# Optimization experiments

Measured on AMD Instinct MI355X. Metric: run time of the kernel, lower is better.

The kernel has to match this reference:

```python
import jax, jax.numpy as jnp
import numpy as np

H = 256      # hidden_dim
MEL = 80     # num_mel
R = 5        # reduction_factor
BS = 128
T_ENC = 512
T_DEC = 1000


def _gru_step(x, h, wih, whh, bih, bhh):
    # PyTorch GRU cell: gates order (r, z, n)
    gi = x @ wih.T + bih            # [bs, 3H]
    gh = h @ whh.T + bhh
    ir, iz, inn = jnp.split(gi, 3, axis=-1)
    hr, hz, hn = jnp.split(gh, 3, axis=-1)
    r = jax.nn.sigmoid(ir + hr)
    z = jax.nn.sigmoid(iz + hz)
    n = jnp.tanh(inn + r * hn)
    return (1.0 - z) * n + z * h


def setup_inputs() -> dict:
    key = jax.random.key(0)
    ks = iter(jax.random.split(key, 40))
    s = 0.05
    def w(shape):
        return jax.random.normal(next(ks), shape, dtype=jnp.float32) * s
    inp = {
        "enc_vec": jax.random.normal(next(ks), (BS, T_ENC, H), dtype=jnp.float32),
        "decoder_input": jax.random.normal(next(ks), (BS, T_DEC, MEL), dtype=jnp.float32),
        # Pre_net
        "pre_w1": w((H, MEL)), "pre_b1": jnp.zeros((H,), jnp.float32),
        "pre_w2": w((H // 2, H)), "pre_b2": jnp.zeros((H // 2,), jnp.float32),
        # Bahdanau attention
        "w1": w((H, H)), "b1": jnp.zeros((H,), jnp.float32),
        "w2": w((H, H)), "b2": jnp.zeros((H,), jnp.float32),
        "v_w": w((1, H)), "v_b": jnp.zeros((1,), jnp.float32),
        # projection and output
        "proj_w": w((H, 2 * H)), "proj_b": jnp.zeros((H,), jnp.float32),
        "out_w": w((MEL * R, H)), "out_b": jnp.zeros((MEL * R,), jnp.float32),
        # Attention GRU (input H//2)
        "att_wih": w((3 * H, H // 2)), "att_whh": w((3 * H, H)),
        "att_bih": jnp.zeros((3 * H,), jnp.float32), "att_bhh": jnp.zeros((3 * H,), jnp.float32),
        # GRU1, GRU2 (input H)
        "g1_wih": w((3 * H, H)), "g1_whh": w((3 * H, H)),
        "g1_bih": jnp.zeros((3 * H,), jnp.float32), "g1_bhh": jnp.zeros((3 * H,), jnp.float32),
        "g2_wih": w((3 * H, H)), "g2_whh": w((3 * H, H)),
        "g2_bih": jnp.zeros((3 * H,), jnp.float32), "g2_bhh": jnp.zeros((3 * H,), jnp.float32),
    }
    return inp


def reference(enc_vec, decoder_input, pre_w1, pre_b1, pre_w2, pre_b2,
              w1, b1, w2, b2, v_w, v_b, proj_w, proj_b, out_w, out_b,
              att_wih, att_whh, att_bih, att_bhh,
              g1_wih, g1_whh, g1_bih, g1_bhh,
              g2_wih, g2_whh, g2_bih, g2_bhh):
    bs = enc_vec.shape[0]
    # Pre_net (dropout omitted -> deterministic eval behavior)
    pre = jax.nn.relu(decoder_input @ pre_w1.T + pre_b1)
    pre = jax.nn.relu(pre @ pre_w2.T + pre_b2)          # [bs, T_dec, H//2]
    steps = decoder_input.shape[1] // R                 # 200
    # teacher-forced inputs: step i uses pre[:, i*R, :]
    xs = jnp.transpose(pre[:, :steps * R:R, :], (1, 0, 2))   # [steps, bs, H//2]
    # hoist W1(enc_vec): constant across decoder steps
    w1enc = enc_vec @ w1.T + b1                         # [bs, T_enc, H]

    h0 = jnp.zeros((bs, H), jnp.float32)

    def step(carry, x):
        ha, h1, h2 = carry
        d = _gru_step(x, ha, att_wih, att_whh, att_bih, att_bhh)   # [bs, H]
        e = jnp.tanh(w1enc + (d @ w2.T + b2)[:, None, :])          # [bs, T_enc, H]
        scores = e @ v_w[0] + v_b[0]                               # [bs, T_enc]
        u = jax.nn.softmax(scores, axis=1)
        d_dot = jnp.einsum('bt,bth->bh', u, enc_vec)               # [bs, H]
        p = jnp.concatenate([d, d_dot], axis=-1) @ proj_w.T + proj_b  # [bs, H]
        o1 = _gru_step(p, h1, g1_wih, g1_whh, g1_bih, g1_bhh)
        in2 = o1 + p
        o2 = _gru_step(in2, h2, g2_wih, g2_whh, g2_bih, g2_bhh)
        out = (in2 + o2) @ out_w.T + out_b                         # [bs, R*MEL]
        return (d, o1, o2), out

    _, ys = jax.lax.scan(step, (h0, h0, h0), xs)        # [steps, bs, R*MEL]
    ys = jnp.transpose(ys, (1, 0, 2)).reshape(bs, steps * R, MEL)
    return ys
```

## Files before the change

### kernel.cpp

```cpp
#include <hip/hip_runtime.h>
#include <hip/hip_bf16.h>

typedef unsigned short u16;
typedef unsigned int   u32;

constexpr int H     = 256;
constexpr int HH    = 128;
constexpr int MELD  = 80;
constexpr int RF    = 5;
constexpr int BS    = 128;
constexpr int TENC  = 512;
constexpr int TDEC  = 1000;
constexpr int STEPS = 200;
constexpr int OD    = 400;
constexpr int M_ALL = STEPS * BS;

constexpr size_t GI_B   = 0;
constexpr size_t ENC16_B= GI_B;
constexpr size_t D16_B  = GI_B   + (size_t)M_ALL*768*4;
constexpr size_t IN2_B  = D16_B;
constexpr size_t W1ET_B = D16_B  + (size_t)M_ALL*512*2;
constexpr size_t P16_B  = W1ET_B;
constexpr size_t IN2H_B = W1ET_B + (size_t)M_ALL*256*2;
constexpr size_t P_B    = W1ET_B + (size_t)BS*H*TENC*2;
constexpr size_t U16_B  = P_B;
constexpr size_t XSH_B  = P_B    + (size_t)M_ALL*256*4;
constexpr size_t ST16_B = XSH_B  + (size_t)M_ALL*128*2;
constexpr size_t WPK_B  = ST16_B + (size_t)M_ALL*256*2;
constexpr size_t WH_B   = WPK_B  + 3*(size_t)393216;
constexpr size_t WH_AW  = 0;
constexpr size_t WH_W2  = WH_AW + 98304*2;
constexpr size_t WH_PJ  = WH_W2 + 65536*2;
constexpr size_t WH_G1  = WH_PJ + 131072*2;
constexpr size_t WH_G2  = WH_G1 + 196608*2;
constexpr size_t WH_OW  = WH_G2 + 196608*2;
constexpr size_t WH_W1  = WH_OW + 102400*2;
constexpr size_t WH_END = WH_W1 + 65536*2;
constexpr size_t NEED_FAST = WH_B + WH_END;

constexpr size_t FBW1E_B  = 65536;
constexpr size_t FBXST_B  = FBW1E_B + (size_t)BS*TENC*H*2;
constexpr size_t FBF32_B  = FBXST_B + (size_t)STEPS*HH*BS*2;
constexpr size_t FBDT_F   = 0;
constexpr size_t FBO1_F   = FBDT_F + 2*(size_t)H*BS;
constexpr size_t FBO2_F   = FBO1_F + 2*(size_t)H*BS;
constexpr size_t FBPT_F   = FBO2_F + 2*(size_t)H*BS;
constexpr size_t FBIN2_F  = FBPT_F + (size_t)H*BS;
constexpr size_t FBST_F   = FBIN2_F + (size_t)H*BS;
constexpr size_t FB_NEED_B = FBF32_B + (FBST_F + 2*(size_t)H*BS) * 4;

__device__ __forceinline__ float bf2f(u16 v) {
  union { u32 x; float f; } c; c.x = ((u32)v) << 16; return c.f;
}
__device__ __forceinline__ float bfu_lo(u32 u) { union { u32 x; float f; } c; c.x = u << 16;        return c.f; }
__device__ __forceinline__ float bfu_hi(u32 u) { union { u32 x; float f; } c; c.x = u & 0xffff0000u; return c.f; }
__device__ __forceinline__ u16 f2bf(float f) {
  union { float f; u32 u; } c; c.f = f;
  u32 u = c.u;
  u32 r = (u + 0x7fffu + ((u >> 16) & 1u)) >> 16;
  return (u16)r;
}
__device__ __forceinline__ u16 f2h(float f) {
  union { _Float16 h; u16 u; } c; c.h = (_Float16)f; return c.u;
}
__device__ __forceinline__ float fexp(float x) {
  return __builtin_amdgcn_exp2f(1.4426950408889634f * x);
}
__device__ __forceinline__ float sigm_f(float x) {
  return __builtin_amdgcn_rcpf(1.0f + __builtin_amdgcn_exp2f(-1.4426950408889634f * x));
}
__device__ __forceinline__ float tanh_f(float x) {
  x = fminf(fmaxf(x, -15.f), 15.f);
  float e = __builtin_amdgcn_exp2f(2.8853900817779268f * x);
  return (e - 1.0f) * __builtin_amdgcn_rcpf(e + 1.0f);
}

typedef _Float16 hlf2 __attribute__((ext_vector_type(2)));
typedef _Float16 f16x8 __attribute__((ext_vector_type(8)));
typedef float f32x4 __attribute__((ext_vector_type(4)));
#if __has_builtin(__builtin_amdgcn_fdot2)
__device__ __forceinline__ float dot2h(float acc, u32 w, u32 h) {
  union { u32 u; hlf2 v; } cw, ch; cw.u = w; ch.u = h;
  return __builtin_amdgcn_fdot2(cw.v, ch.v, acc, false);
}
#else
__device__ __forceinline__ float dot2h(float acc, u32 w, u32 h) {
  union { u32 u; _Float16 f[2]; } cw, ch; cw.u = w; ch.u = h;
  return acc + (float)cw.f[0] * (float)ch.f[0] + (float)cw.f[1] * (float)ch.f[1];
}
#endif
__device__ __forceinline__ void dot8h(float& acc, const uint4 w, const uint4 hp) {
  acc = dot2h(acc, w.x, hp.x);
  acc = dot2h(acc, w.y, hp.y);
  acc = dot2h(acc, w.z, hp.z);
  acc = dot2h(acc, w.w, hp.w);
}

__global__ __launch_bounds__(256) void k_zero(float* __restrict__ out, int n) {
  int i = blockIdx.x * 256 + threadIdx.x;
  if (i < n) out[i] = 0.f;
}


__global__ __launch_bounds__(256) void k_prenet_f(
    const float* __restrict__ dec, const float* __restrict__ w1, const float* __restrict__ b1,
    const float* __restrict__ w2, const float* __restrict__ b2, u16* __restrict__ xsh)
{
  const int s = blockIdx.x, tid = threadIdx.x;
  __shared__ float X0[32][80];
  __shared__ float P1t[32][256];
  for (int bt = 0; bt < 4; ++bt) {
    const int b0 = bt * 32;
    __syncthreads();
    for (int i = tid; i < 32 * 80; i += 256) {
      int bb = i / 80, m = i - bb * 80;
      X0[bb][m] = dec[((size_t)(b0 + bb) * TDEC + (size_t)s * RF) * MELD + m];
    }
    __syncthreads();
    {
      const int h = tid;
      float acc[32];
      const float bias = b1[h];
      #pragma unroll
      for (int r = 0; r < 32; ++r) acc[r] = bias;
      const float* wr = w1 + (size_t)h * MELD;
      for (int m = 0; m < 80; m += 4) {
        float4 wv = *(const float4*)(wr + m);
        #pragma unroll
        for (int r = 0; r < 32; ++r) {
          float4 x = *(const float4*)&X0[r][m];
          acc[r] += x.x * wv.x + x.y * wv.y + x.z * wv.z + x.w * wv.w;
        }
      }
      #pragma unroll
      for (int r = 0; r < 32; ++r) P1t[r][h] = fmaxf(acc[r], 0.f);
    }
    __syncthreads();
    {
      const int k = tid & 127, bh = tid >> 7;
      float acc[16];
      const float bias = b2[k];
      #pragma unroll
      for (int r = 0; r < 16; ++r) acc[r] = bias;
      const float* wr = w2 + (size_t)k * H;
      for (int h = 0; h < H; h += 4) {
        float4 wv = *(const float4*)(wr + h);
        #pragma unroll
        for (int r = 0; r < 16; ++r) {
          float4 x = *(const float4*)&P1t[bh * 16 + r][h];
          acc[r] += x.x * wv.x + x.y * wv.y + x.z * wv.z + x.w * wv.w;
        }
      }
      #pragma unroll
      for (int r = 0; r < 16; ++r)
        xsh[((size_t)s * BS + b0 + bh * 16 + r) * HH + k] = f2h(fmaxf(acc[r], 0.f));
    }
  }
}

__global__ __launch_bounds__(256) void k_packall(
    const float* __restrict__ enc, u16* __restrict__ enc16,
    const float* __restrict__ awhh, const float* __restrict__ g1whh,
    const float* __restrict__ g2whh, u32* __restrict__ wpk,
    const float* __restrict__ awih, u16* __restrict__ awih16,
    const float* __restrict__ w2w,  u16* __restrict__ w2w16,
    const float* __restrict__ pjw,  u16* __restrict__ pjw16,
    const float* __restrict__ g1wih, u16* __restrict__ g1w16,
    const float* __restrict__ g2wih, u16* __restrict__ g2w16,
    const float* __restrict__ ow,   u16* __restrict__ ow16,
    const float* __restrict__ w1w,  u16* __restrict__ w1w16)
{
  int i = blockIdx.x * 256 + threadIdx.x;
  if (i < 16777216) { enc16[i] = f2h(enc[i]); return; }
  i -= 16777216;
  if (i < 294912) {
    int which = i / 98304, idx = i - which * 98304;
    const float* w = which == 0 ? awhh : (which == 1 ? g1whh : g2whh);
    int ii = idx & 3;
    int j  = (idx >> 2) & 255;
    int k4 = (idx >> 10) & 31;
    int g  = idx >> 15;
    int k2 = 4 * k4 + ii;
    union { _Float16 f[2]; u32 u; } c;
    c.f[0] = (_Float16)w[((size_t)g * 256 + j) * 256 + 2 * k2];
    c.f[1] = (_Float16)w[((size_t)g * 256 + j) * 256 + 2 * k2 + 1];
    wpk[which * 98304 + idx] = c.u;
    return;
  }
  i -= 294912;
  if (i < 98304)  { awih16[i] = f2h(awih[i]); return; }  i -= 98304;
  if (i < 65536)  { w2w16[i]  = f2h(w2w[i]);  return; }  i -= 65536;
  if (i < 131072) { pjw16[i]  = f2h(pjw[i]);  return; }  i -= 131072;
  if (i < 196608) { g1w16[i]  = f2h(g1wih[i]); return; } i -= 196608;
  if (i < 196608) { g2w16[i]  = f2h(g2wih[i]); return; } i -= 196608;
  if (i < 102400) { ow16[i]   = f2h(ow[i]);   return; }  i -= 102400;
  if (i < 65536)  { w1w16[i]  = f2h(w1w[i]);  return; }
}
constexpr int PACKALL_N = 16777216 + 294912 + 856064;

__global__ __launch_bounds__(256) void k_hgemm(
    const u16* __restrict__ A, int lda,
    const u16* __restrict__ W, int K,
    const float* __restrict__ bias,
    float* __restrict__ C, u16* __restrict__ Ch, int ldc, int N,
    float* __restrict__ outmap, u16* __restrict__ CbfT)
{
  __shared__ _Float16 As[128 * 40];
  __shared__ _Float16 Ws[64 * 40];
  const int m0 = blockIdx.y * 128, n0 = blockIdx.x * 64;
  const int tid = threadIdx.x;
  const int wv = tid >> 6, lane = tid & 63;
  const int l15 = lane & 15, hi = lane >> 4;
  f32x4 acc[2][4];
  #pragma unroll
  for (int mi = 0; mi < 2; ++mi)
    #pragma unroll
    for (int ni = 0; ni < 4; ++ni) acc[mi][ni] = (f32x4){0.f, 0.f, 0.f, 0.f};

  const int ar = tid >> 1, ac = (tid & 1) * 16;
  const int wr = tid >> 2, wc = (tid & 3) * 8;
  for (int k0 = 0; k0 < K; k0 += 32) {
    __syncthreads();
    {
      const u16* src = A + (size_t)(m0 + ar) * lda + k0 + ac;
      uint4 v0 = *(const uint4*)(src);
      uint4 v1 = *(const uint4*)(src + 8);
      *(uint4*)&As[ar * 40 + ac] = v0;
      *(uint4*)&As[ar * 40 + ac + 8] = v1;
    }
    {
      uint4 v;
      if (n0 + wr < N) v = *(const uint4*)(W + (size_t)(n0 + wr) * K + k0 + wc);
      else { v.x = v.y = v.z = v.w = 0u; }
      *(uint4*)&Ws[wr * 40 + wc] = v;
    }
    __syncthreads();
    f16x8 af[2], bf[4];
    #pragma unroll
    for (int mi = 0; mi < 2; ++mi)
      af[mi] = *(const f16x8*)&As[(wv * 32 + mi * 16 + l15) * 40 + hi * 8];
    #pragma unroll
    for (int ni = 0; ni < 4; ++ni)
      bf[ni] = *(const f16x8*)&Ws[(ni * 16 + l15) * 40 + hi * 8];
    #pragma unroll
    for (int mi = 0; mi < 2; ++mi)
      #pragma unroll
      for (int ni = 0; ni < 4; ++ni)
        acc[mi][ni] = __builtin_amdgcn_mfma_f32_16x16x32_f16(af[mi], bf[ni], acc[mi][ni], 0, 0, 0);
  }
  const int gm = m0 + wv * 32;
  #pragma unroll
  for (int ni = 0; ni < 4; ++ni) {
    const int col = n0 + ni * 16 + l15;
    if (col < N) {
      const float bv = bias[col];
      #pragma unroll
      for (int mi = 0; mi < 2; ++mi) {
        #pragma unroll
        for (int r = 0; r < 4; ++r) {
          const int row = gm + mi * 16 + hi * 4 + r;
          float v = acc[mi][ni][r] + bv;
          if (outmap) {
            int s = row >> 7, b = row & 127;
            int fr = s * RF + col / MELD, mel = col - (col / MELD) * MELD;
            outmap[((size_t)b * TDEC + fr) * MELD + mel] = v;
          } else if (CbfT) {
            float a = fminf(fmaxf(2.8853900817779268f * v, -15.f), 15.f);
            CbfT[(((size_t)(row >> 9) * 256 + col) << 9) + (row & 511)] =
                f2bf(__builtin_amdgcn_exp2f(a));
          } else {
            if (C)  C[(size_t)row * ldc + col] = v;
            if (Ch) Ch[(size_t)row * ldc + col] = f2h(v);
          }
        }
      }
    }
  }
}

__global__ __launch_bounds__(256) void k_ddgemm(
    const u16* __restrict__ U, const float* __restrict__ enc,
    u16* __restrict__ D16)
{
  __shared__ _Float16 As[128 * 40];
  __shared__ _Float16 Ws[64 * 40];
  const int b = blockIdx.z;
  const int m0 = blockIdx.y * 128, n0 = blockIdx.x * 64;
  const int tid = threadIdx.x;
  const int wv = tid >> 6, lane = tid & 63;
  const int l15 = lane & 15, hi = lane >> 4;
  f32x4 acc[2][4];
  #pragma unroll
  for (int mi = 0; mi < 2; ++mi)
    #pragma unroll
    for (int ni = 0; ni < 4; ++ni) acc[mi][ni] = (f32x4){0.f, 0.f, 0.f, 0.f};

  const u16* A = U + (size_t)b * STEPS * TENC;
  const float* E = enc + (size_t)b * TENC * H;
  const int ar = tid >> 1, ac = (tid & 1) * 16;
  for (int k0 = 0; k0 < TENC; k0 += 32) {
    __syncthreads();
    {
      const u16* src = A + (size_t)(m0 + ar) * TENC + k0 + ac;
      uint4 v0 = *(const uint4*)(src);
      uint4 v1 = *(const uint4*)(src + 8);
      *(uint4*)&As[ar * 40 + ac] = v0;
      *(uint4*)&As[ar * 40 + ac + 8] = v1;
    }
    {
      #pragma unroll
      for (int it = 0; it < 2; ++it) {
        int flat = tid + it * 256;
        int kk = flat >> 4, hc4 = (flat & 15) * 4;
        float4 v = *(const float4*)(E + (size_t)(k0 + kk) * H + n0 + hc4);
        Ws[(hc4 + 0) * 40 + kk] = (_Float16)v.x;
        Ws[(hc4 + 1) * 40 + kk] = (_Float16)v.y;
        Ws[(hc4 + 2) * 40 + kk] = (_Float16)v.z;
        Ws[(hc4 + 3) * 40 + kk] = (_Float16)v.w;
      }
    }
    __syncthreads();
    f16x8 af[2], bf[4];
    #pragma unroll
    for (int mi = 0; mi < 2; ++mi)
      af[mi] = *(const f16x8*)&As[(wv * 32 + mi * 16 + l15) * 40 + hi * 8];
    #pragma unroll
    for (int ni = 0; ni < 4; ++ni)
      bf[ni] = *(const f16x8*)&Ws[(ni * 16 + l15) * 40 + hi * 8];
    #pragma unroll
    for (int mi = 0; mi < 2; ++mi)
      #pragma unroll
      for (int ni = 0; ni < 4; ++ni)
        acc[mi][ni] = __builtin_amdgcn_mfma_f32_16x16x32_f16(af[mi], bf[ni], acc[mi][ni], 0, 0, 0);
  }
  const int gm = m0 + wv * 32;
  #pragma unroll
  for (int ni = 0; ni < 4; ++ni) {
    const int col = n0 + ni * 16 + l15;
    #pragma unroll
    for (int mi = 0; mi < 2; ++mi) {
      #pragma unroll
      for (int r = 0; r < 4; ++r) {
        const int row = gm + mi * 16 + hi * 4 + r;
        if (row < STEPS)
          D16[((size_t)(row * BS + b)) * 512 + 256 + col] = f2h(acc[mi][ni][r]);
      }
    }
  }
}

constexpr int KC4H = 2;
constexpr int RG4H = 14;
__global__ __launch_bounds__(512) void k_chain(
    const float* __restrict__ gi,
    const uint4* __restrict__ wpk4,
    const float* __restrict__ bhh,
    const float* __restrict__ addsrc,
    int astride,
    float* __restrict__ outp, int ostride,
    u16* __restrict__ outph, int ostrideh)
{
  const int b = blockIdx.x, tid = threadIdx.x;
  const int j = tid & 255, kh = tid >> 8;
  __shared__ __align__(16) _Float16 hf[256];
  __shared__ float psum[3][256];
  __shared__ uint4 wl4[3][2 * KC4H][256];
  for (int i = tid; i < 3 * 2 * KC4H * 256; i += 512) {
    int g = i / (2 * KC4H * 256), rem = i - g * (2 * KC4H * 256);
    int slot = rem >> 8, jj = rem & 255;
    int c = slot < KC4H ? slot : slot - KC4H;
    int k4 = (slot < KC4H ? 0 : 16) + c;
    wl4[g][slot][jj] = wpk4[((size_t)g * 32 + k4) * 256 + jj];
  }
  uint4 wreg[3][RG4H];
  #pragma unroll
  for (int g = 0; g < 3; ++g) {
    #pragma unroll
    for (int t = 0; t < RG4H; ++t) {
      const int k4 = kh * 16 + KC4H + t;
      wreg[g][t] = wpk4[((size_t)g * 32 + k4) * 256 + j];
    }
  }
  if (tid < 256) hf[tid] = (_Float16)0.f;
  float hreg = 0.f;
  const float br = bhh[j], bz = bhh[256 + j], bn = bhh[512 + j];
  float gr = 0.f, gz = 0.f, gn = 0.f, av = 0.f;
  if (kh == 0) {
    const float* gim = gi + (size_t)b * 768;
    gr = gim[j]; gz = gim[256 + j]; gn = gim[512 + j];
    if (addsrc) av = addsrc[(size_t)b * astride + j];
  }
  __syncthreads();
  for (int s = 0; s < STEPS; ++s) {
    float gr_n = 0.f, gz_n = 0.f, gn_n = 0.f, av_n = 0.f;
    if (kh == 0 && s + 1 < STEPS) {
      const size_t mn = (size_t)(s + 1) * BS + b;
      const float* gim = gi + mn * 768;
      gr_n = gim[j]; gz_n = gim[256 + j]; gn_n = gim[512 + j];
      if (addsrc) av_n = addsrc[mn * astride + j];
    }
    float ar = 0.f, az = 0.f, an = 0.f;
    const int k4b = kh * 16;
    #pragma unroll
    for (int t = 0; t < RG4H; ++t) {
      const int k4 = k4b + KC4H + t;
      uint4 hp = *(const uint4*)&hf[8 * k4];
      dot8h(ar, wreg[0][t], hp); dot8h(az, wreg[1][t], hp); dot8h(an, wreg[2][t], hp);
    }
    #pragma unroll
    for (int c = 0; c < KC4H; ++c) {
      const int k4 = k4b + c;
      const int slot = kh * KC4H + c;
      uint4 hp = *(const uint4*)&hf[8 * k4];
      dot8h(ar, wl4[0][slot][j], hp); dot8h(az, wl4[1][slot][j], hp); dot8h(an, wl4[2][slot][j], hp);
    }
    if (kh == 1) { psum[0][j] = ar; psum[1][j] = az; psum[2][j] = an; }
    __syncthreads();
    if (kh == 0) {
      const size_t m = (size_t)s * BS + b;
      ar += psum[0][j]; az += psum[1][j]; an += psum[2][j];
      float r = sigm_f(gr + ar + br);
      float z = sigm_f(gz + az + bz);
      float n = tanh_f(gn + r * (an + bn));
      float hn_ = (1.f - z) * n + z * hreg;
      hreg = hn_;
      hf[j] = (_Float16)hn_;
      float ov = hn_ + av;
      if (outp)  outp[m * ostride + j] = ov;
      if (outph) outph[m * ostrideh + j] = f2h(ov);
    }
    __syncthreads();
    gr = gr_n; gz = gz_n; gn = gn_n; av = av_n;
  }
}

constexpr int ATT_ST = 10;
__global__ __launch_bounds__(256) void k_att(
    const u16* __restrict__ w1eT, const float* __restrict__ Q,
    const float* __restrict__ vw_, u16* __restrict__ U16)
{
  const int b = blockIdx.x, s0 = blockIdx.y * ATT_ST, tid = threadIdx.x;
  __shared__ float qt[ATT_ST][260];
  __shared__ float vws[256];
  __shared__ float redw[ATT_ST][4];
  vws[tid] = -2.0f * vw_[tid];
  #pragma unroll
  for (int si = 0; si < ATT_ST; ++si) {
    float q = 2.8853900817779268f * Q[((size_t)(s0 + si) * BS + b) * H + tid];
    qt[si][tid] = __builtin_amdgcn_exp2f(fminf(fmaxf(q, -15.f), 15.f));
  }
  __syncthreads();

  float sc0[ATT_ST], sc1[ATT_ST];
  #pragma unroll
  for (int si = 0; si < ATT_ST; ++si) { sc0[si] = 0.f; sc1[si] = 0.f; }
  const u32* wrow = (const u32*)w1eT + (size_t)b * H * (TENC / 2);
  for (int h = 0; h < H; h += 4) {
    u32 wa = wrow[(size_t)(h + 0) * 256 + tid];
    u32 wb = wrow[(size_t)(h + 1) * 256 + tid];
    u32 wc = wrow[(size_t)(h + 2) * 256 + tid];
    u32 wd = wrow[(size_t)(h + 3) * 256 + tid];
    float Ea0 = bfu_lo(wa), Ea1 = bfu_hi(wa);
    float Eb0 = bfu_lo(wb), Eb1 = bfu_hi(wb);
    float Ec0 = bfu_lo(wc), Ec1 = bfu_hi(wc);
    float Ed0 = bfu_lo(wd), Ed1 = bfu_hi(wd);
    float4 vv = *(const float4*)&vws[h];
    #pragma unroll
    for (int si = 0; si < ATT_ST; ++si) {
      float4 Eq = *(const float4*)&qt[si][h];
      {
        float F1 = __builtin_fmaf(Ea0, Eq.x, 1.f);
        float F2 = __builtin_fmaf(Eb0, Eq.y, 1.f);
        float F3 = __builtin_fmaf(Ec0, Eq.z, 1.f);
        float F4 = __builtin_fmaf(Ed0, Eq.w, 1.f);
        float P12 = F1 * F2, P34 = F3 * F4;
        float u12 = __builtin_fmaf(vv.y, F1, vv.x * F2);
        float u34 = __builtin_fmaf(vv.w, F3, vv.z * F4);
        float num = __builtin_fmaf(P12, u34, P34 * u12);
        sc0[si] = __builtin_fmaf(num, __builtin_amdgcn_rcpf(P12 * P34), sc0[si]);
      }
      {
        float F1 = __builtin_fmaf(Ea1, Eq.x, 1.f);
        float F2 = __builtin_fmaf(Eb1, Eq.y, 1.f);
        float F3 = __builtin_fmaf(Ec1, Eq.z, 1.f);
        float F4 = __builtin_fmaf(Ed1, Eq.w, 1.f);
        float P12 = F1 * F2, P34 = F3 * F4;
        float u12 = __builtin_fmaf(vv.y, F1, vv.x * F2);
        float u34 = __builtin_fmaf(vv.w, F3, vv.z * F4);
        float num = __builtin_fmaf(P12, u34, P34 * u12);
        sc1[si] = __builtin_fmaf(num, __builtin_amdgcn_rcpf(P12 * P34), sc1[si]);
      }
    }
  }
  const int lane = tid & 63, wvi = tid >> 6;
  #pragma unroll
  for (int si = 0; si < ATT_ST; ++si) {
    float mw = fmaxf(sc0[si], sc1[si]);
    for (int off = 1; off < 64; off <<= 1) mw = fmaxf(mw, __shfl_xor(mw, off));
    if (lane == 0) redw[si][wvi] = mw;
  }
  __syncthreads();
  #pragma unroll
  for (int si = 0; si < ATT_ST; ++si) {
    float mx = fmaxf(fmaxf(redw[si][0], redw[si][1]), fmaxf(redw[si][2], redw[si][3]));
    sc0[si] = fexp(sc0[si] - mx);
    sc1[si] = fexp(sc1[si] - mx);
  }
  __syncthreads();
  #pragma unroll
  for (int si = 0; si < ATT_ST; ++si) {
    float sm = sc0[si] + sc1[si];
    for (int off = 1; off < 64; off <<= 1) sm += __shfl_xor(sm, off);
    if (lane == 0) redw[si][wvi] = sm;
  }
  __syncthreads();
  #pragma unroll
  for (int si = 0; si < ATT_ST; ++si) {
    float tot = redw[si][0] + redw[si][1] + redw[si][2] + redw[si][3];
    float li = __builtin_amdgcn_rcpf(tot);
    u32 pk = (u32)f2h(sc0[si] * li) | ((u32)f2h(sc1[si] * li) << 16);
    *(u32*)&U16[((size_t)b * STEPS + s0 + si) * TENC + 2 * tid] = pk;
  }
}

__global__ __launch_bounds__(256) void fbk_zeroinit(float* __restrict__ fst) {
  int i = blockIdx.x * 256 + threadIdx.x;
  if (i < H * BS)              fst[FBDT_F + i] = 0.f;
  else if (i < 2 * H * BS)     fst[FBO1_F + (i - H * BS)] = 0.f;
  else if (i < 3 * H * BS)     fst[FBO2_F + (i - 2 * H * BS)] = 0.f;
}

__global__ __launch_bounds__(256) void fbk_prenet(
    const float* __restrict__ dec, const float* __restrict__ w1, const float* __restrict__ b1,
    const float* __restrict__ w2, const float* __restrict__ b2, u16* __restrict__ xsT)
{
  const int s = blockIdx.x, tid = threadIdx.x;
  __shared__ float X0[32][80];
  __shared__ float P1t[32][256];
  for (int bt = 0; bt < 4; ++bt) {
    const int b0 = bt * 32;
    __syncthreads();
    for (int i = tid; i < 32 * 80; i += 256) {
      int bb = i / 80, m = i - bb * 80;
      X0[bb][m] = dec[((size_t)(b0 + bb) * TDEC + (size_t)s * RF) * MELD + m];
    }
    __syncthreads();
    {
      const int h = tid;
      float acc[32];
      const float bias = b1[h];
      #pragma unroll
      for (int r = 0; r < 32; ++r) acc[r] = bias;
      const float* wr = w1 + (size_t)h * MELD;
      for (int m = 0; m < 80; m += 4) {
        float4 wv = *(const float4*)(wr + m);
        #pragma unroll
        for (int r = 0; r < 32; ++r) {
          float4 x = *(const float4*)&X0[r][m];
          acc[r] += x.x * wv.x + x.y * wv.y + x.z * wv.z + x.w * wv.w;
        }
      }
      #pragma unroll
      for (int r = 0; r < 32; ++r) P1t[r][h] = fmaxf(acc[r], 0.f);
    }
    __syncthreads();
    {
      const int k = tid & 127, bh = tid >> 7;
      float acc[16];
      const float bias = b2[k];
      #pragma unroll
      for (int r = 0; r < 16; ++r) acc[r] = bias;
      const float* wr = w2 + (size_t)k * H;
      for (int h = 0; h < H; h += 4) {
        float4 wv = *(const float4*)(wr + h);
        #pragma unroll
        for (int r = 0; r < 16; ++r) {
          float4 x = *(const float4*)&P1t[bh * 16 + r][h];
          acc[r] += x.x * wv.x + x.y * wv.y + x.z * wv.z + x.w * wv.w;
        }
      }
      #pragma unroll
      for (int r = 0; r < 16; ++r)
        xsT[((size_t)s * HH + k) * BS + b0 + bh * 16 + r] = f2bf(fmaxf(acc[r], 0.f));
    }
  }
}

__global__ __launch_bounds__(256) void fbk_w1enc(
    const float* __restrict__ enc, const float* __restrict__ w1, const float* __restrict__ b1,
    u16* __restrict__ w1e)
{
  const int row0 = blockIdx.x * 32;
  const int tid = threadIdx.x;
  __shared__ float A[32 * 256];
  for (int i = tid * 4; i < 32 * 256; i += 256 * 4) {
    float4 v = *(const float4*)(enc + (size_t)row0 * H + i);
    A[i] = v.x; A[i + 1] = v.y; A[i + 2] = v.z; A[i + 3] = v.w;
  }
  __syncthreads();
  const int h = tid;
  float acc[32];
  const float bias = b1[h];
  #pragma unroll
  for (int r = 0; r < 32; ++r) acc[r] = bias;
  const float* wr = w1 + (size_t)h * H;
  for (int k = 0; k < H; k += 4) {
    float4 wv = *(const float4*)(wr + k);
    #pragma unroll
    for (int r = 0; r < 32; ++r) {
      float4 a = *(const float4*)&A[r * 256 + k];
      acc[r] += a.x * wv.x + a.y * wv.y + a.z * wv.z + a.w * wv.w;
    }
  }
  #pragma unroll
  for (int r = 0; r < 32; ++r) w1e[((size_t)row0 + r) * H + h] = f2bf(acc[r]);
}

__device__ __forceinline__ void fb_gru_body(
    float (*w6)[260], float (*pA)[128], float (*pB)[128], int j, int tid,
    const float* __restrict__ gi_src, const float* __restrict__ h_src,
    const float* __restrict__ wih, const float* __restrict__ whh,
    const float* __restrict__ bih, const float* __restrict__ bhh,
    float* __restrict__ h_out, float* __restrict__ sum_out)
{
  for (int i = tid; i < 3 * H; i += 256) {
    int gg = i >> 8, k = i & 255;
    w6[gg][k]     = wih[((size_t)gg * H + j) * H + k];
    w6[3 + gg][k] = whh[((size_t)gg * H + j) * H + k];
  }
  __syncthreads();
  const int b = tid & 127, kh = tid >> 7;
  float pr = 0, pz = 0, pn = 0, hr = 0, hz = 0, hn = 0;
  for (int k = kh * 128; k < kh * 128 + 128; k += 4) {
    float4 wia = *(const float4*)&w6[0][k];
    float4 wib = *(const float4*)&w6[1][k];
    float4 wic = *(const float4*)&w6[2][k];
    float4 wha = *(const float4*)&w6[3][k];
    float4 whb = *(const float4*)&w6[4][k];
    float4 whc = *(const float4*)&w6[5][k];
    float x0 = gi_src[(size_t)(k + 0) * BS + b], x1 = gi_src[(size_t)(k + 1) * BS + b];
    float x2 = gi_src[(size_t)(k + 2) * BS + b], x3 = gi_src[(size_t)(k + 3) * BS + b];
    float h0 = h_src[(size_t)(k + 0) * BS + b],  h1 = h_src[(size_t)(k + 1) * BS + b];
    float h2 = h_src[(size_t)(k + 2) * BS + b],  h3 = h_src[(size_t)(k + 3) * BS + b];
    pr += x0 * wia.x + x1 * wia.y + x2 * wia.z + x3 * wia.w;
    pz += x0 * wib.x + x1 * wib.y + x2 * wib.z + x3 * wib.w;
    pn += x0 * wic.x + x1 * wic.y + x2 * wic.z + x3 * wic.w;
    hr += h0 * wha.x + h1 * wha.y + h2 * wha.z + h3 * wha.w;
    hz += h0 * whb.x + h1 * whb.y + h2 * whb.z + h3 * whb.w;
    hn += h0 * whc.x + h1 * whc.y + h2 * whc.z + h3 * whc.w;
  }
  if (kh) {
    pA[0][b] = pr; pA[1][b] = pz; pA[2][b] = pn;
    pB[0][b] = hr; pB[1][b] = hz; pB[2][b] = hn;
  }
  __syncthreads();
  if (!kh) {
    float gir = pr + pA[0][b] + bih[j];
    float giz = pz + pA[1][b] + bih[H + j];
    float gin = pn + pA[2][b] + bih[2 * H + j];
    float ghr = hr + pB[0][b] + bhh[j];
    float ghz = hz + pB[1][b] + bhh[H + j];
    float ghn = hn + pB[2][b] + bhh[2 * H + j];
    float r = sigm_f(gir + ghr);
    float z = sigm_f(giz + ghz);
    float n = tanh_f(gin + r * ghn);
    float hp = h_src[(size_t)j * BS + b];
    float o = (1.f - z) * n + z * hp;
    h_out[(size_t)j * BS + b] = o;
    if (sum_out) sum_out[(size_t)j * BS + b] = o + gi_src[(size_t)j * BS + b];
  }
}

__global__ __launch_bounds__(256) void fbk_attgru(
    const u16* __restrict__ xstu, float* __restrict__ fst,
    const float* __restrict__ awih, const float* __restrict__ awhh,
    const float* __restrict__ abih, const float* __restrict__ abhh, int s)
{
  const int j = blockIdx.x, tid = threadIdx.x;
  __shared__ float w6[6][260];
  __shared__ float pA[3][128];
  __shared__ float pB[3][128];
  const float* dprev = fst + FBDT_F + (size_t)(s & 1) * H * BS;
  float*       dcur  = fst + FBDT_F + (size_t)((s + 1) & 1) * H * BS;
  for (int i = tid; i < 3 * HH; i += 256) {
    int gg = i >> 7, k = i & (HH - 1);
    w6[gg][k] = awih[((size_t)gg * H + j) * HH + k];
  }
  for (int i = tid; i < 3 * H; i += 256) {
    int gg = i >> 8, k = i & (H - 1);
    w6[3 + gg][k] = awhh[((size_t)gg * H + j) * H + k];
  }
  __syncthreads();
  const u16* xcol = xstu + (size_t)s * HH * BS;
  const int b = tid & 127, kh = tid >> 7;
  float pr = 0, pz = 0, pn = 0, hr = 0, hz = 0, hn = 0;
  for (int k = kh * 64; k < kh * 64 + 64; k += 4) {
    float4 wa = *(const float4*)&w6[0][k];
    float4 wb = *(const float4*)&w6[1][k];
    float4 wc = *(const float4*)&w6[2][k];
    float x0 = bf2f(xcol[(size_t)(k + 0) * BS + b]), x1 = bf2f(xcol[(size_t)(k + 1) * BS + b]);
    float x2 = bf2f(xcol[(size_t)(k + 2) * BS + b]), x3 = bf2f(xcol[(size_t)(k + 3) * BS + b]);
    pr += x0 * wa.x + x1 * wa.y + x2 * wa.z + x3 * wa.w;
    pz += x0 * wb.x + x1 * wb.y + x2 * wb.z + x3 * wb.w;
    pn += x0 * wc.x + x1 * wc.y + x2 * wc.z + x3 * wc.w;
  }
  for (int k = kh * 128; k < kh * 128 + 128; k += 4) {
    float4 wa = *(const float4*)&w6[3][k];
    float4 wb = *(const float4*)&w6[4][k];
    float4 wc = *(const float4*)&w6[5][k];
    float h0 = dprev[(size_t)(k + 0) * BS + b], h1 = dprev[(size_t)(k + 1) * BS + b];
    float h2 = dprev[(size_t)(k + 2) * BS + b], h3 = dprev[(size_t)(k + 3) * BS + b];
    hr += h0 * wa.x + h1 * wa.y + h2 * wa.z + h3 * wa.w;
    hz += h0 * wb.x + h1 * wb.y + h2 * wb.z + h3 * wb.w;
    hn += h0 * wc.x + h1 * wc.y + h2 * wc.z + h3 * wc.w;
  }
  if (kh) {
    pA[0][b] = pr; pA[1][b] = pz; pA[2][b] = pn;
    pB[0][b] = hr; pB[1][b] = hz; pB[2][b] = hn;
  }
  __syncthreads();
  if (!kh) {
    float gir = pr + pA[0][b] + abih[j];
    float giz = pz + pA[1][b] + abih[H + j];
    float gin = pn + pA[2][b] + abih[2 * H + j];
    float ghr = hr + pB[0][b] + abhh[j];
    float ghz = hz + pB[1][b] + abhh[H + j];
    float ghn = hn + pB[2][b] + abhh[2 * H + j];
    float r = sigm_f(gir + ghr);
    float z = sigm_f(giz + ghz);
    float n = tanh_f(gin + r * ghn);
    float hp = dprev[(size_t)j * BS + b];
    dcur[(size_t)j * BS + b] = (1.f - z) * n + z * hp;
  }
}

__global__ __launch_bounds__(256) void fbk_attn(
    const float* __restrict__ enc, const u16* __restrict__ w1eu,
    const float* __restrict__ w2w, const float* __restrict__ b2w,
    const float* __restrict__ vww, const float* __restrict__ vbw,
    const float* __restrict__ pjw, const float* __restrict__ pjb,
    float* __restrict__ fst, int s)
{
  const int b3 = blockIdx.x, tid = threadIdx.x;
  __shared__ float dsh[256], qs[256], ddh[256], vwsh[256], ev[512], red[256];
  const float* dcur = fst + FBDT_F + (size_t)((s + 1) & 1) * H * BS;
  float* pT = fst + FBPT_F;
  dsh[tid]  = dcur[(size_t)tid * BS + b3];
  vwsh[tid] = vww[tid];
  __syncthreads();
  {
    const int jj = tid;
    const float* wr = w2w + (size_t)jj * H;
    float acc = b2w[jj];
    for (int k = 0; k < H; k += 8) {
      float4 wA = *(const float4*)(wr + k);
      float4 wB = *(const float4*)(wr + k + 4);
      float4 dA = *(const float4*)&dsh[k];
      float4 dB = *(const float4*)&dsh[k + 4];
      acc += dA.x * wA.x + dA.y * wA.y + dA.z * wA.z + dA.w * wA.w
           + dB.x * wB.x + dB.y * wB.y + dB.z * wB.z + dB.w * wB.w;
    }
    qs[jj] = acc;
  }
  __syncthreads();
  const float vbf = vbw[0];
  const u16* wr0 = w1eu + ((size_t)b3 * TENC + tid) * H;
  const u16* wr1 = wr0 + (size_t)256 * H;
  float sc0 = vbf, sc1 = vbf;
  for (int h = 0; h < H; h += 8) {
    uint4 ua = *(const uint4*)(wr0 + h);
    uint4 uc = *(const uint4*)(wr1 + h);
    float4 qA = *(const float4*)&qs[h];
    float4 qB = *(const float4*)&qs[h + 4];
    float4 vA = *(const float4*)&vwsh[h];
    float4 vB = *(const float4*)&vwsh[h + 4];
    sc0 += vA.x * tanh_f(bfu_lo(ua.x) + qA.x) + vA.y * tanh_f(bfu_hi(ua.x) + qA.y)
         + vA.z * tanh_f(bfu_lo(ua.y) + qA.z) + vA.w * tanh_f(bfu_hi(ua.y) + qA.w)
         + vB.x * tanh_f(bfu_lo(ua.z) + qB.x) + vB.y * tanh_f(bfu_hi(ua.z) + qB.y)
         + vB.z * tanh_f(bfu_lo(ua.w) + qB.z) + vB.w * tanh_f(bfu_hi(ua.w) + qB.w);
    sc1 += vA.x * tanh_f(bfu_lo(uc.x) + qA.x) + vA.y * tanh_f(bfu_hi(uc.x) + qA.y)
         + vA.z * tanh_f(bfu_lo(uc.y) + qA.z) + vA.w * tanh_f(bfu_hi(uc.y) + qA.w)
         + vB.x * tanh_f(bfu_lo(uc.z) + qB.x) + vB.y * tanh_f(bfu_hi(uc.z) + qB.y)
         + vB.z * tanh_f(bfu_lo(uc.w) + qB.z) + vB.w * tanh_f(bfu_hi(uc.w) + qB.w);
  }
  red[tid] = fmaxf(sc0, sc1);
  __syncthreads();
  for (int off = 128; off > 0; off >>= 1) {
    if (tid < off) red[tid] = fmaxf(red[tid], red[tid + off]);
    __syncthreads();
  }
  float mx = red[0];
  __syncthreads();
  float e0 = fexp(sc0 - mx), e1 = fexp(sc1 - mx);
  ev[tid] = e0; ev[256 + tid] = e1;
  red[tid] = e0 + e1;
  __syncthreads();
  for (int off = 128; off > 0; off >>= 1) {
    if (tid < off) red[tid] += red[tid + off];
    __syncthreads();
  }
  float linv = __builtin_amdgcn_rcpf(red[0]);
  __syncthreads();
  {
    float vacc = 0.f;
    const float* ep = enc + (size_t)b3 * TENC * H + tid;
    for (int tt = 0; tt < TENC; tt += 4) {
      float4 e4 = *(const float4*)&ev[tt];
      vacc += e4.x * ep[(size_t)(tt + 0) * H] + e4.y * ep[(size_t)(tt + 1) * H]
            + e4.z * ep[(size_t)(tt + 2) * H] + e4.w * ep[(size_t)(tt + 3) * H];
    }
    ddh[tid] = vacc * linv;
  }
  __syncthreads();
  {
    const int jj = tid;
    const float* wr = pjw + (size_t)jj * (2 * H);
    float acc = pjb[jj];
    for (int k = 0; k < H; k += 8) {
      float4 wA = *(const float4*)(wr + k);
      float4 wB = *(const float4*)(wr + k + 4);
      float4 dA = *(const float4*)&dsh[k];
      float4 dB = *(const float4*)&dsh[k + 4];
      acc += dA.x * wA.x + dA.y * wA.y + dA.z * wA.z + dA.w * wA.w
           + dB.x * wB.x + dB.y * wB.y + dB.z * wB.z + dB.w * wB.w;
    }
    for (int k = 0; k < H; k += 8) {
      float4 wA = *(const float4*)(wr + H + k);
      float4 wB = *(const float4*)(wr + H + k + 4);
      float4 dA = *(const float4*)&ddh[k];
      float4 dB = *(const float4*)&ddh[k + 4];
      acc += dA.x * wA.x + dA.y * wA.y + dA.z * wA.z + dA.w * wA.w
           + dB.x * wB.x + dB.y * wB.y + dB.z * wB.z + dB.w * wB.w;
    }
    pT[(size_t)jj * BS + b3] = acc;
  }
}

__global__ __launch_bounds__(256) void fbk_gru1(
    float* __restrict__ fst,
    const float* __restrict__ wih, const float* __restrict__ whh,
    const float* __restrict__ bih, const float* __restrict__ bhh, int s)
{
  __shared__ float w6[6][260];
  __shared__ float pA[3][128];
  __shared__ float pB[3][128];
  const float* pT     = fst + FBPT_F;
  const float* o1prev = fst + FBO1_F + (size_t)(s & 1) * H * BS;
  float*       o1cur  = fst + FBO1_F + (size_t)((s + 1) & 1) * H * BS;
  float*       in2T   = fst + FBIN2_F;
  fb_gru_body(w6, pA, pB, blockIdx.x, threadIdx.x, pT, o1prev, wih, whh, bih, bhh, o1cur, in2T);
}

__device__ __forceinline__ void fb_out_body(
    float (*pA)[128], int bb, int tid, int s,
    const float* __restrict__ sT, const float* __restrict__ ow,
    const float* __restrict__ ob, float* __restrict__ out)
{
  const int b = tid & 127, kh = tid >> 7;
  for (int r = bb; r < OD; r += 128) {
    const float* wr = ow + (size_t)r * H + kh * 128;
    float acc = 0.f;
    for (int kk = 0; kk < 128; kk += 4) {
      float4 wv = *(const float4*)(wr + kk);
      const float* sp = sT + (size_t)(kh * 128 + kk) * BS + b;
      acc += sp[0] * wv.x + sp[BS] * wv.y + sp[2 * BS] * wv.z + sp[3 * BS] * wv.w;
    }
    __syncthreads();
    if (kh) pA[0][b] = acc;
    __syncthreads();
    if (!kh) {
      float y = acc + pA[0][b] + ob[r];
      int frame = s * RF + r / MELD;
      int m = r - (r / MELD) * MELD;
      out[((size_t)b * TDEC + frame) * MELD + m] = y;
    }
  }
}

__global__ __launch_bounds__(256) void fbk_gru2out(
    float* __restrict__ fst,
    const float* __restrict__ wih, const float* __restrict__ whh,
    const float* __restrict__ bih, const float* __restrict__ bhh,
    const float* __restrict__ ow, const float* __restrict__ ob,
    float* __restrict__ out, int s)
{
  const int bid = blockIdx.x, tid = threadIdx.x;
  __shared__ float w6[6][260];
  __shared__ float pA[3][128];
  __shared__ float pB[3][128];
  if (bid < 256) {
    const float* in2T   = fst + FBIN2_F;
    const float* o2prev = fst + FBO2_F + (size_t)(s & 1) * H * BS;
    float*       o2cur  = fst + FBO2_F + (size_t)((s + 1) & 1) * H * BS;
    float*       stp    = fst + FBST_F + (size_t)(s & 1) * H * BS;
    fb_gru_body(w6, pA, pB, bid, tid, in2T, o2prev, wih, whh, bih, bhh, o2cur, stp);
  } else if (s > 0) {
    const float* sT = fst + FBST_F + (size_t)((s - 1) & 1) * H * BS;
    fb_out_body(pA, bid - 256, tid, s - 1, sT, ow, ob, out);
  }
}

__global__ __launch_bounds__(256) void fbk_outlast(
    const float* __restrict__ fst, const float* __restrict__ ow,
    const float* __restrict__ ob, float* __restrict__ out)
{
  __shared__ float pA[3][128];
  const float* sT = fst + FBST_F + (size_t)((STEPS - 1) & 1) * H * BS;
  fb_out_body(pA, blockIdx.x, threadIdx.x, STEPS - 1, sT, ow, ob, out);
}

extern "C" void kernel_launch(void* const* d_in, const int* in_sizes, int n_in,
                              void* d_out, int out_size, void* d_ws, size_t ws_size,
                              hipStream_t stream) {
  const float* enc   = (const float*)d_in[0];
  const float* dec   = (const float*)d_in[1];
  const float* pw1   = (const float*)d_in[2];
  const float* pb1   = (const float*)d_in[3];
  const float* pw2   = (const float*)d_in[4];
  const float* pb2   = (const float*)d_in[5];
  const float* w1w   = (const float*)d_in[6];
  const float* b1w   = (const float*)d_in[7];
  const float* w2w   = (const float*)d_in[8];
  const float* b2w   = (const float*)d_in[9];
  const float* vww   = (const float*)d_in[10];
  const float* vbw   = (const float*)d_in[11];
  const float* pjw   = (const float*)d_in[12];
  const float* pjb   = (const float*)d_in[13];
  const float* ow    = (const float*)d_in[14];
  const float* ob    = (const float*)d_in[15];
  const float* awih  = (const float*)d_in[16];
  const float* awhh  = (const float*)d_in[17];
  const float* abih  = (const float*)d_in[18];
  const float* abhh  = (const float*)d_in[19];
  const float* g1wih = (const float*)d_in[20];
  const float* g1whh = (const float*)d_in[21];
  const float* g1bih = (const float*)d_in[22];
  const float* g1bhh = (const float*)d_in[23];
  const float* g2wih = (const float*)d_in[24];
  const float* g2whh = (const float*)d_in[25];
  const float* g2bih = (const float*)d_in[26];
  const float* g2bhh = (const float*)d_in[27];
  float* out = (float*)d_out;
  char* wsb = (char*)d_ws;

  if (ws_size >= NEED_FAST) {
    float* GI   = (float*)(wsb + GI_B);
    u16*   ENC16= (u16*)(wsb + ENC16_B);
    u16*   D16  = (u16*)(wsb + D16_B);
    float* IN2  = (float*)(wsb + IN2_B);
    u16*   w1eT = (u16*)(wsb + W1ET_B);
    u16*   P16  = (u16*)(wsb + P16_B);
    u16*   IN2H = (u16*)(wsb + IN2H_B);
    float* P    = (float*)(wsb + P_B);
    u16*   U16  = (u16*)(wsb + U16_B);
    u16*   XSH  = (u16*)(wsb + XSH_B);
    u16*   ST16 = (u16*)(wsb + ST16_B);
    u32*   wpkA = (u32*)(wsb + WPK_B);
    u32*   wpk1 = wpkA + 98304;
    u32*   wpk2 = wpk1 + 98304;
    u16*   awih16 = (u16*)(wsb + WH_B + WH_AW);
    u16*   w2w16  = (u16*)(wsb + WH_B + WH_W2);
    u16*   pjw16  = (u16*)(wsb + WH_B + WH_PJ);
    u16*   g1w16  = (u16*)(wsb + WH_B + WH_G1);
    u16*   g2w16  = (u16*)(wsb + WH_B + WH_G2);
    u16*   ow16   = (u16*)(wsb + WH_B + WH_OW);
    u16*   w1w16  = (u16*)(wsb + WH_B + WH_W1);

    k_packall<<<PACKALL_N / 256, 256, 0, stream>>>(
        enc, ENC16, awhh, g1whh, g2whh, wpkA,
        awih, awih16, w2w, w2w16, pjw, pjw16, g1wih, g1w16,
        g2wih, g2w16, ow, ow16, w1w, w1w16);
    k_hgemm<<<dim3(4, (BS * TENC) / 128), 256, 0, stream>>>(
        ENC16, H, w1w16, H, b1w, nullptr, nullptr, 0, 256, nullptr, w1eT);
    k_prenet_f<<<STEPS, 256, 0, stream>>>(dec, pw1, pb1, pw2, pb2, XSH);
    k_hgemm<<<dim3(12, M_ALL / 128), 256, 0, stream>>>(XSH, HH, awih16, HH, abih, GI, nullptr, 768, 768, nullptr, nullptr);
    k_chain<<<BS, 512, 0, stream>>>(GI, (const uint4*)wpkA, abhh, nullptr, 0, nullptr, 0, D16, 512);
    k_hgemm<<<dim3(4, M_ALL / 128), 256, 0, stream>>>(D16, 512, w2w16, H, b2w, GI, nullptr, 256, 256, nullptr, nullptr);
    k_att<<<dim3(BS, STEPS / ATT_ST), 256, 0, stream>>>(w1eT, GI, vww, U16);
    k_ddgemm<<<dim3(4, 2, BS), 256, 0, stream>>>(U16, enc, D16);
    k_hgemm<<<dim3(4, M_ALL / 128), 256, 0, stream>>>(D16, 512, pjw16, 2 * H, pjb, P, P16, 256, 256, nullptr, nullptr);
    k_hgemm<<<dim3(12, M_ALL / 128), 256, 0, stream>>>(P16, H, g1w16, H, g1bih, GI, nullptr, 768, 768, nullptr, nullptr);
    k_chain<<<BS, 512, 0, stream>>>(GI, (const uint4*)wpk1, g1bhh, P, 256, IN2, 256, IN2H, 256);
    k_hgemm<<<dim3(12, M_ALL / 128), 256, 0, stream>>>(IN2H, H, g2w16, H, g2bih, GI, nullptr, 768, 768, nullptr, nullptr);
    k_chain<<<BS, 512, 0, stream>>>(GI, (const uint4*)wpk2, g2bhh, IN2, 256, nullptr, 0, ST16, 256);
    k_hgemm<<<dim3(7, M_ALL / 128), 256, 0, stream>>>(ST16, H, ow16, H, ob, nullptr, nullptr, 0, OD, out, nullptr);
    return;
  }

  if (ws_size < FB_NEED_B) {
    k_zero<<<(out_size + 255) / 256, 256, 0, stream>>>(out, out_size);
    return;
  }

  u16*  w1eu = (u16*)(wsb + FBW1E_B);
  u16*  xstu = (u16*)(wsb + FBXST_B);
  float* fst = (float*)(wsb + FBF32_B);

  fbk_zeroinit<<<384, 256, 0, stream>>>(fst);
  fbk_prenet<<<STEPS, 256, 0, stream>>>(dec, pw1, pb1, pw2, pb2, xstu);
  fbk_w1enc<<<(BS * TENC) / 32, 256, 0, stream>>>(enc, w1w, b1w, w1eu);
  for (int s = 0; s < STEPS; ++s) {
    fbk_attgru<<<256, 256, 0, stream>>>(xstu, fst, awih, awhh, abih, abhh, s);
    fbk_attn<<<BS, 256, 0, stream>>>(enc, w1eu, w2w, b2w, vww, vbw, pjw, pjb, fst, s);
    fbk_gru1<<<256, 256, 0, stream>>>(fst, g1wih, g1whh, g1bih, g1bhh, s);
    fbk_gru2out<<<384, 256, 0, stream>>>(fst, g2wih, g2whh, g2bih, g2bhh, ow, ob, out, s);
  }
  fbk_outlast<<<BS, 256, 0, stream>>>(fst, ow, ob, out);
}
```

Before: 1.615 ms.

## Compute GRU chain recurrent matvec with MFMA using broadcast hidden state

Replaces the per-thread fdot2 recurrent matvec in the sequential GRU chain kernel with MFMA 16x16x32 instructions. The weights are repacked into B-fragment layout and held in registers across 8 waves. The hidden vector is broadcast as the A operand, and only row 0 of each result is used. This removes the split-K partial-sum reduction and the LDS weight spill. In exchange it wastes 15/16 of the MFMA rows and adds a gsh shared-memory gather on the latency-bound per-step critical path.

```diff
diff --git a/kernel.cpp b/kernel.cpp
--- a/kernel.cpp
+++ b/kernel.cpp
@@ -78,23 +78,6 @@
 typedef _Float16 hlf2 __attribute__((ext_vector_type(2)));
 typedef _Float16 f16x8 __attribute__((ext_vector_type(8)));
 typedef float f32x4 __attribute__((ext_vector_type(4)));
-#if __has_builtin(__builtin_amdgcn_fdot2)
-__device__ __forceinline__ float dot2h(float acc, u32 w, u32 h) {
-  union { u32 u; hlf2 v; } cw, ch; cw.u = w; ch.u = h;
-  return __builtin_amdgcn_fdot2(cw.v, ch.v, acc, false);
-}
-#else
-__device__ __forceinline__ float dot2h(float acc, u32 w, u32 h) {
-  union { u32 u; _Float16 f[2]; } cw, ch; cw.u = w; ch.u = h;
-  return acc + (float)cw.f[0] * (float)ch.f[0] + (float)cw.f[1] * (float)ch.f[1];
-}
-#endif
-__device__ __forceinline__ void dot8h(float& acc, const uint4 w, const uint4 hp) {
-  acc = dot2h(acc, w.x, hp.x);
-  acc = dot2h(acc, w.y, hp.y);
-  acc = dot2h(acc, w.z, hp.z);
-  acc = dot2h(acc, w.w, hp.w);
-}
 
 __global__ __launch_bounds__(256) void k_zero(float* __restrict__ out, int n) {
   int i = blockIdx.x * 256 + threadIdx.x;
@@ -176,14 +159,15 @@
   if (i < 294912) {
     int which = i / 98304, idx = i - which * 98304;
     const float* w = which == 0 ? awhh : (which == 1 ? g1whh : g2whh);
-    int ii = idx & 3;
-    int j  = (idx >> 2) & 255;
-    int k4 = (idx >> 10) & 31;
-    int g  = idx >> 15;
-    int k2 = 4 * k4 + ii;
+    int q  = idx & 3;
+    int l  = (idx >> 2) & 63;
+    int kt = (idx >> 8) & 7;
+    int nt = idx >> 11;
+    int col = nt * 16 + (l & 15);
+    int k   = kt * 32 + (l >> 4) * 8 + 2 * q;
     union { _Float16 f[2]; u32 u; } c;
-    c.f[0] = (_Float16)w[((size_t)g * 256 + j) * 256 + 2 * k2];
-    c.f[1] = (_Float16)w[((size_t)g * 256 + j) * 256 + 2 * k2 + 1];
+    c.f[0] = (_Float16)w[(size_t)col * 256 + k];
+    c.f[1] = (_Float16)w[(size_t)col * 256 + k + 1];
     wpk[which * 98304 + idx] = c.u;
     return;
   }
@@ -349,11 +333,9 @@
   }
 }
 
-constexpr int KC4H = 2;
-constexpr int RG4H = 14;
 __global__ __launch_bounds__(512) void k_chain(
     const float* __restrict__ gi,
-    const uint4* __restrict__ wpk4,
+    const uint4* __restrict__ wpkB,
     const float* __restrict__ bhh,
     const float* __restrict__ addsrc,
     int astride,
@@ -361,64 +343,54 @@
     u16* __restrict__ outph, int ostrideh)
 {
   const int b = blockIdx.x, tid = threadIdx.x;
-  const int j = tid & 255, kh = tid >> 8;
+  const int wv = tid >> 6, lane = tid & 63;
+  const int l15 = lane & 15, hi = lane >> 4;
   __shared__ __align__(16) _Float16 hf[256];
-  __shared__ float psum[3][256];
-  __shared__ uint4 wl4[3][2 * KC4H][256];
-  for (int i = tid; i < 3 * 2 * KC4H * 256; i += 512) {
-    int g = i / (2 * KC4H * 256), rem = i - g * (2 * KC4H * 256);
-    int slot = rem >> 8, jj = rem & 255;
-    int c = slot < KC4H ? slot : slot - KC4H;
-    int k4 = (slot < KC4H ? 0 : 16) + c;
-    wl4[g][slot][jj] = wpk4[((size_t)g * 32 + k4) * 256 + jj];
-  }
-  uint4 wreg[3][RG4H];
-  #pragma unroll
-  for (int g = 0; g < 3; ++g) {
-    #pragma unroll
-    for (int t = 0; t < RG4H; ++t) {
-      const int k4 = kh * 16 + KC4H + t;
-      wreg[g][t] = wpk4[((size_t)g * 32 + k4) * 256 + j];
-    }
-  }
+  __shared__ float gsh[768];
+  f16x8 bfrag[6][8];
+  #pragma unroll
+  for (int nti = 0; nti < 6; ++nti)
+    #pragma unroll
+    for (int kt = 0; kt < 8; ++kt)
+      bfrag[nti][kt] = *(const f16x8*)&wpkB[(((size_t)(wv * 6 + nti) * 8 + kt) * 64 + lane)];
   if (tid < 256) hf[tid] = (_Float16)0.f;
-  float hreg = 0.f;
-  const float br = bhh[j], bz = bhh[256 + j], bn = bhh[512 + j];
+  const int j = tid;
+  float br = 0.f, bz = 0.f, bn = 0.f, hreg = 0.f;
   float gr = 0.f, gz = 0.f, gn = 0.f, av = 0.f;
-  if (kh == 0) {
+  if (tid < 256) {
+    br = bhh[j]; bz = bhh[256 + j]; bn = bhh[512 + j];
     const float* gim = gi + (size_t)b * 768;
     gr = gim[j]; gz = gim[256 + j]; gn = gim[512 + j];
     if (addsrc) av = addsrc[(size_t)b * astride + j];
   }
   __syncthreads();
   for (int s = 0; s < STEPS; ++s) {
+    f32x4 acc[6];
+    #pragma unroll
+    for (int nti = 0; nti < 6; ++nti) acc[nti] = (f32x4){0.f, 0.f, 0.f, 0.f};
+    #pragma unroll
+    for (int kt = 0; kt < 8; ++kt) {
+      f16x8 af = *(const f16x8*)&hf[kt * 32 + hi * 8];
+      #pragma unroll
+      for (int nti = 0; nti < 6; ++nti)
+        acc[nti] = __builtin_amdgcn_mfma_f32_16x16x32_f16(af, bfrag[nti][kt], acc[nti], 0, 0, 0);
+    }
     float gr_n = 0.f, gz_n = 0.f, gn_n = 0.f, av_n = 0.f;
-    if (kh == 0 && s + 1 < STEPS) {
+    if (tid < 256 && s + 1 < STEPS) {
       const size_t mn = (size_t)(s + 1) * BS + b;
       const float* gim = gi + mn * 768;
       gr_n = gim[j]; gz_n = gim[256 + j]; gn_n = gim[512 + j];
       if (addsrc) av_n = addsrc[mn * astride + j];
     }
-    float ar = 0.f, az = 0.f, an = 0.f;
-    const int k4b = kh * 16;
-    #pragma unroll
-    for (int t = 0; t < RG4H; ++t) {
-      const int k4 = k4b + KC4H + t;
-      uint4 hp = *(const uint4*)&hf[8 * k4];
-      dot8h(ar, wreg[0][t], hp); dot8h(az, wreg[1][t], hp); dot8h(an, wreg[2][t], hp);
-    }
-    #pragma unroll
-    for (int c = 0; c < KC4H; ++c) {
-      const int k4 = k4b + c;
-      const int slot = kh * KC4H + c;
-      uint4 hp = *(const uint4*)&hf[8 * k4];
-      dot8h(ar, wl4[0][slot][j], hp); dot8h(az, wl4[1][slot][j], hp); dot8h(an, wl4[2][slot][j], hp);
-    }
-    if (kh == 1) { psum[0][j] = ar; psum[1][j] = az; psum[2][j] = an; }
-    __syncthreads();
-    if (kh == 0) {
+    if (hi == 0) {
+      #pragma unroll
+      for (int nti = 0; nti < 6; ++nti)
+        gsh[(wv * 6 + nti) * 16 + l15] = acc[nti][0];
+    }
+    __syncthreads();
+    if (tid < 256) {
       const size_t m = (size_t)s * BS + b;
-      ar += psum[0][j]; az += psum[1][j]; an += psum[2][j];
+      float ar = gsh[j], az = gsh[256 + j], an = gsh[512 + j];
       float r = sigm_f(gr + ar + br);
       float z = sigm_f(gz + az + bz);
       float n = tanh_f(gn + r * (an + bn));
```

New measurement: 1.568 ms. -2.9%, faster.
